# Optimization experiments

Hardware: AMD Instinct MI355X
Metric: run time of the kernel (lower is better)

Reference implementation:

```python
import jax, jax.numpy as jnp
import numpy as np

N_VERTS = 600_000
N_TETS = 1_000_000

TRI_TABLE = np.array([
    [-1,-1,-1,-1,-1,-1],[1,0,2,-1,-1,-1],[4,0,3,-1,-1,-1],[1,4,2,1,3,4],
    [3,1,5,-1,-1,-1],[2,3,0,2,5,3],[1,4,0,1,5,4],[4,2,5,-1,-1,-1],
    [4,5,2,-1,-1,-1],[4,1,0,4,5,1],[3,2,0,3,5,2],[1,3,5,-1,-1,-1],
    [4,1,2,4,3,1],[3,0,4,-1,-1,-1],[2,0,1,-1,-1,-1],[-1,-1,-1,-1,-1,-1]], dtype=np.int32)
NUM_TRI_TABLE = np.array([0,1,1,2,1,2,2,1,1,2,2,1,2,1,1,0], dtype=np.int32)
BASE_TET_EDGES = np.array([0,1,0,2,0,3,1,2,1,3,2,3], dtype=np.int64)


def setup_inputs() -> dict:
    rng = np.random.default_rng(0)
    tet = rng.integers(0, N_VERTS, size=(N_TETS, 4), dtype=np.int64)
    # static edge-unique structure (depends only on integer connectivity)
    edges = np.sort(tet[:, BASE_TET_EDGES].reshape(-1, 2), axis=1)  # (T*6, 2)
    uniq, inv = np.unique(edges, axis=0, return_inverse=True)
    key = jax.random.key(0)
    k1, k2 = jax.random.split(key)
    pos_nx3 = jax.random.normal(k1, (N_VERTS, 3), dtype=jnp.float32)
    sdf_n = jax.random.normal(k2, (N_VERTS,), dtype=jnp.float32)
    return {
        'pos_nx3': pos_nx3,
        'sdf_n': sdf_n,
        'tet_fx4': jnp.asarray(tet, dtype=jnp.int32),
        'unique_edges': jnp.asarray(uniq, dtype=jnp.int32),
        'idx_map': jnp.asarray(inv.reshape(-1, 6), dtype=jnp.int32),
    }


def reference(pos_nx3, sdf_n, tet_fx4, unique_edges, idx_map):
    tri_table = jnp.asarray(TRI_TABLE)
    num_tri_table = jnp.asarray(NUM_TRI_TABLE)
    T = tet_fx4.shape[0]

    occ_n = sdf_n > 0.0                              # (N,)
    occ_fx4 = occ_n[tet_fx4]                         # (T,4)
    occ_sum = occ_fx4.sum(-1)                        # (T,)
    valid = (occ_sum > 0) & (occ_sum < 4)            # (T,) surface tets

    # --- per-unique-edge interpolation (padded: all edges, masked) ---
    e_occ = occ_n[unique_edges]                      # (Eu,2)
    crossing = e_occ[:, 0] != e_occ[:, 1]            # sign change on edge
    s = sdf_n[unique_edges]                          # (Eu,2)
    p = pos_nx3[unique_edges]                        # (Eu,2,3)
    denom = s[:, 0] - s[:, 1]
    denom = jnp.where(crossing, denom, jnp.ones_like(denom))
    w0 = -s[:, 1] / denom                            # weight for endpoint 0
    w1 = s[:, 0] / denom                             # weight for endpoint 1
    verts = p[:, 0] * w0[:, None] + p[:, 1] * w1[:, None]
    verts = jnp.where(crossing[:, None], verts, jnp.zeros_like(verts))  # (Eu,3)

    # --- triangle table lookup (faces index the full unique-edge array) ---
    v_id = jnp.array([1, 2, 4, 8], dtype=jnp.int32)
    tetindex = (occ_fx4.astype(jnp.int32) * v_id).sum(-1)      # (T,) in [0,16)
    n_tri = num_tri_table[tetindex]                            # (T,) 0/1/2
    tri = tri_table[tetindex]                                  # (T,6) local edge ids, -1 pad
    face_idx = jnp.take_along_axis(idx_map, jnp.clip(tri, 0, 5), axis=1)
    face_idx = face_idx.reshape(T, 2, 3)
    tri_valid = valid[:, None] & (jnp.arange(2, dtype=jnp.int32)[None, :] < n_tri[:, None])
    faces = jnp.where(tri_valid[..., None], face_idx, -1)      # (T,2,3)

    # --- UV atlas (map_uv), static size ---
    Ngrid = int(np.ceil(np.sqrt((2 * T + 1) // 2)))
    lin = jnp.linspace(0.0, 1.0 - 1.0 / Ngrid, Ngrid, dtype=jnp.float32)
    tex_y, tex_x = jnp.meshgrid(lin, lin, indexing='ij')
    pad = 0.9 / Ngrid
    uvs = jnp.stack([tex_x, tex_y, tex_x + pad, tex_y,
                     tex_x + pad, tex_y + pad, tex_x, tex_y + pad], axis=-1).reshape(-1, 2)
    tet_gidx = jnp.arange(T, dtype=jnp.int32)
    tet_idx = (tet_gidx % Ngrid) + (tet_gidx // Ngrid) * Ngrid  # _idx()
    tri_i = jnp.arange(2, dtype=jnp.int32)[None, :]
    base = tet_idx[:, None] * 4                                 # (T,1)
    uv_idx = jnp.stack([jnp.broadcast_to(base, (T, 2)),
                        base + tri_i + 1,
                        base + tri_i + 2], axis=-1)             # (T,2,3)
    uv_idx = jnp.where(tri_valid[..., None], uv_idx, -1)
    return verts, faces, uvs, uv_idx
```

## Files before the change

### kernel.cpp

```cpp
#include <hip/hip_runtime.h>
#include <math.h>

__constant__ int c_tri_table[16][6] = {
    {-1,-1,-1,-1,-1,-1},{1,0,2,-1,-1,-1},{4,0,3,-1,-1,-1},{1,4,2,1,3,4},
    {3,1,5,-1,-1,-1},{2,3,0,2,5,3},{1,4,0,1,5,4},{4,2,5,-1,-1,-1},
    {4,5,2,-1,-1,-1},{4,1,0,4,5,1},{3,2,0,3,5,2},{1,3,5,-1,-1,-1},
    {4,1,2,4,3,1},{3,0,4,-1,-1,-1},{2,0,1,-1,-1,-1},{-1,-1,-1,-1,-1,-1}};
__constant__ int c_num_tri[16] = {0,1,1,2,1,2,2,1,1,2,2,1,2,1,1,0};

__global__ void dmtet_verts_kernel(const float* __restrict__ pos,
                                   const float* __restrict__ sdf,
                                   const int2* __restrict__ edges,
                                   float* __restrict__ verts, int Eu) {
    int stride = gridDim.x * blockDim.x;
    for (int e = blockIdx.x * blockDim.x + threadIdx.x; e < Eu; e += stride) {
        int2 ed = edges[e];
        float s0 = sdf[ed.x];
        float s1 = sdf[ed.y];
        bool crossing = (s0 > 0.0f) != (s1 > 0.0f);
        float denom = crossing ? (s0 - s1) : 1.0f;
        float w0 = -s1 / denom;
        float w1 =  s0 / denom;
        const float* p0 = pos + 3LL * ed.x;
        const float* p1 = pos + 3LL * ed.y;
        float ox = crossing ? (p0[0] * w0 + p1[0] * w1) : 0.0f;
        float oy = crossing ? (p0[1] * w0 + p1[1] * w1) : 0.0f;
        float oz = crossing ? (p0[2] * w0 + p1[2] * w1) : 0.0f;
        long long o = 3LL * e;
        verts[o + 0] = ox;
        verts[o + 1] = oy;
        verts[o + 2] = oz;
    }
}

__global__ void dmtet_tets_kernel(const float* __restrict__ sdf,
                                  const int4* __restrict__ tets,
                                  const int2* __restrict__ idx_map,
                                  float* __restrict__ faces_out,
                                  float* __restrict__ uvidx_out, int T) {
    int stride = gridDim.x * blockDim.x;
    for (int t = blockIdx.x * blockDim.x + threadIdx.x; t < T; t += stride) {
        int4 v = tets[t];
        int idx = (sdf[v.x] > 0.0f ? 1 : 0) | (sdf[v.y] > 0.0f ? 2 : 0) |
                  (sdf[v.z] > 0.0f ? 4 : 0) | (sdf[v.w] > 0.0f ? 8 : 0);
        int  ntri  = c_num_tri[idx];
        bool valid = (idx != 0) && (idx != 15);

        int2 a = idx_map[3LL * t + 0];
        int2 b = idx_map[3LL * t + 1];
        int2 c = idx_map[3LL * t + 2];
        int im[6] = {a.x, a.y, b.x, b.y, c.x, c.y};

        long long o = 6LL * t;
        #pragma unroll
        for (int j = 0; j < 6; ++j) {
            bool tv = valid && ((j < 3) ? (ntri > 0) : (ntri > 1));
            int tri = c_tri_table[idx][j];
            int cl = tri < 0 ? 0 : tri;
            faces_out[o + j] = (float)(tv ? im[cl] : -1);
        }

        int base = 4 * t;
        bool tv0 = valid && (ntri > 0);
        bool tv1 = valid && (ntri > 1);
        uvidx_out[o + 0] = tv0 ? (float)(base)     : -1.0f;
        uvidx_out[o + 1] = tv0 ? (float)(base + 1) : -1.0f;
        uvidx_out[o + 2] = tv0 ? (float)(base + 2) : -1.0f;
        uvidx_out[o + 3] = tv1 ? (float)(base)     : -1.0f;
        uvidx_out[o + 4] = tv1 ? (float)(base + 2) : -1.0f;
        uvidx_out[o + 5] = tv1 ? (float)(base + 3) : -1.0f;
    }
}

__global__ void dmtet_uvs_kernel(float2* __restrict__ uvs, int Ngrid,
                                 int total, float step, float pad) {
    int stride = gridDim.x * blockDim.x;
    for (int k = blockIdx.x * blockDim.x + threadIdx.x; k < total; k += stride) {
        int q = k >> 2;
        int j = k & 3;
        int gx = q % Ngrid;
        int gy = q / Ngrid;
        float x = (float)gx * step;
        float y = (float)gy * step;
        float u = (j == 1 || j == 2) ? x + pad : x;
        float w = (j >= 2) ? y + pad : y;
        uvs[k] = make_float2(u, w);
    }
}

extern "C" void kernel_launch(void* const* d_in, const int* in_sizes, int n_in,
                              void* d_out, int out_size, void* d_ws, size_t ws_size,
                              hipStream_t stream) {
    const float* pos     = (const float*)d_in[0];
    const float* sdf     = (const float*)d_in[1];
    const int*   tet     = (const int*)d_in[2];
    const int*   edges   = (const int*)d_in[3];
    const int*   idx_map = (const int*)d_in[4];

    int T  = in_sizes[2] / 4;
    int Eu = in_sizes[3] / 2;

    long long half = (2LL * T + 1) / 2;
    int Ngrid = (int)ceil(sqrt((double)half));
    while ((long long)Ngrid * Ngrid < half) Ngrid++;
    while ((long long)(Ngrid - 1) * (Ngrid - 1) >= half) Ngrid--;

    float* out   = (float*)d_out;
    float* verts = out;
    float* faces = verts + 3LL * Eu;
    float* uvs   = faces + 6LL * T;
    float* uvidx = uvs   + 8LL * Ngrid * Ngrid;

    float step = (float)((1.0 - 1.0 / (double)Ngrid) / (double)(Ngrid - 1));
    float pad  = 0.9f / (float)Ngrid;

    const int BLK = 256;
    auto nblk = [&](long long n) {
        long long b = (n + BLK - 1) / BLK;
        return (int)(b > 16384 ? 16384 : b);
    };

    dmtet_verts_kernel<<<nblk(Eu), BLK, 0, stream>>>(
        pos, sdf, (const int2*)edges, verts, Eu);

    dmtet_tets_kernel<<<nblk(T), BLK, 0, stream>>>(
        sdf, (const int4*)tet, (const int2*)idx_map, faces, uvidx, T);

    int total_uv = Ngrid * Ngrid * 4;
    dmtet_uvs_kernel<<<nblk(total_uv), BLK, 0, stream>>>(
        (float2*)uvs, Ngrid, total_uv, step, pad);
}
```

Baseline: 349.8 us.

## Vectorize loads and stores, add nontemporal hints, two edges per thread

The vertex kernel now handles two edges per thread with a 16-byte edge load and computes one reciprocal per edge instead of two divides. The tet kernel loads idx_map as one 16-byte plus one 8-byte access. The UV kernel writes 16-byte float4 values. All streaming loads and stores use nontemporal builtins, and the grid-stride loops become one-shot launches. The goal is fewer memory instructions and less cache pollution on a bandwidth-bound workload. The risks are slightly different rounding from the reciprocal multiply and a possible alignment problem on the v2i load of idx_map.

```diff
diff --git a/kernel.cpp b/kernel.cpp
--- a/kernel.cpp
+++ b/kernel.cpp
@@ -1,5 +1,10 @@
 #include <hip/hip_runtime.h>
 #include <math.h>
+
+typedef int   v2i __attribute__((ext_vector_type(2)));
+typedef int   v4i __attribute__((ext_vector_type(4)));
+typedef float v2f __attribute__((ext_vector_type(2)));
+typedef float v4f __attribute__((ext_vector_type(4)));
 
 __constant__ int c_tri_table[16][6] = {
     {-1,-1,-1,-1,-1,-1},{1,0,2,-1,-1,-1},{4,0,3,-1,-1,-1},{1,4,2,1,3,4},
@@ -8,84 +13,117 @@
     {4,1,2,4,3,1},{3,0,4,-1,-1,-1},{2,0,1,-1,-1,-1},{-1,-1,-1,-1,-1,-1}};
 __constant__ int c_num_tri[16] = {0,1,1,2,1,2,2,1,1,2,2,1,2,1,1,0};
 
-__global__ void dmtet_verts_kernel(const float* __restrict__ pos,
-                                   const float* __restrict__ sdf,
-                                   const int2* __restrict__ edges,
-                                   float* __restrict__ verts, int Eu) {
-    int stride = gridDim.x * blockDim.x;
-    for (int e = blockIdx.x * blockDim.x + threadIdx.x; e < Eu; e += stride) {
-        int2 ed = edges[e];
-        float s0 = sdf[ed.x];
-        float s1 = sdf[ed.y];
-        bool crossing = (s0 > 0.0f) != (s1 > 0.0f);
-        float denom = crossing ? (s0 - s1) : 1.0f;
-        float w0 = -s1 / denom;
-        float w1 =  s0 / denom;
-        const float* p0 = pos + 3LL * ed.x;
-        const float* p1 = pos + 3LL * ed.y;
-        float ox = crossing ? (p0[0] * w0 + p1[0] * w1) : 0.0f;
-        float oy = crossing ? (p0[1] * w0 + p1[1] * w1) : 0.0f;
-        float oz = crossing ? (p0[2] * w0 + p1[2] * w1) : 0.0f;
-        long long o = 3LL * e;
-        verts[o + 0] = ox;
-        verts[o + 1] = oy;
-        verts[o + 2] = oz;
+__global__ void __launch_bounds__(256) dmtet_verts_kernel(
+        const float* __restrict__ pos,
+        const float* __restrict__ sdf,
+        const int* __restrict__ edges,
+        float* __restrict__ verts, int Eu) {
+    int t = blockIdx.x * blockDim.x + threadIdx.x;
+    int e0 = 2 * t;
+    if (e0 >= Eu) return;
+
+    int ax, ay, bx, by;
+    bool have2 = (e0 + 1 < Eu);
+    if (have2) {
+        v4i ed = __builtin_nontemporal_load((const v4i*)(edges + 2 * e0));
+        ax = ed.x; ay = ed.y; bx = ed.z; by = ed.w;
+    } else {
+        v2i ed = __builtin_nontemporal_load((const v2i*)(edges + 2 * e0));
+        ax = ed.x; ay = ed.y; bx = ed.x; by = ed.y;
+    }
+
+    float sa0 = sdf[ax], sa1 = sdf[ay];
+    float sb0 = sdf[bx], sb1 = sdf[by];
+    const float* pa0 = pos + 3LL * ax;
+    const float* pa1 = pos + 3LL * ay;
+    const float* pb0 = pos + 3LL * bx;
+    const float* pb1 = pos + 3LL * by;
+    float a0x = pa0[0], a0y = pa0[1], a0z = pa0[2];
+    float a1x = pa1[0], a1y = pa1[1], a1z = pa1[2];
+    float b0x = pb0[0], b0y = pb0[1], b0z = pb0[2];
+    float b1x = pb1[0], b1y = pb1[1], b1z = pb1[2];
+
+    bool ca = (sa0 > 0.0f) != (sa1 > 0.0f);
+    float da = ca ? (sa0 - sa1) : 1.0f;
+    float ia = 1.0f / da;
+    float wa0 = -sa1 * ia, wa1 = sa0 * ia;
+    float ox0 = ca ? (a0x * wa0 + a1x * wa1) : 0.0f;
+    float oy0 = ca ? (a0y * wa0 + a1y * wa1) : 0.0f;
+    float oz0 = ca ? (a0z * wa0 + a1z * wa1) : 0.0f;
+
+    bool cb = (sb0 > 0.0f) != (sb1 > 0.0f);
+    float db = cb ? (sb0 - sb1) : 1.0f;
+    float ib = 1.0f / db;
+    float wb0 = -sb1 * ib, wb1 = sb0 * ib;
+    float ox1 = cb ? (b0x * wb0 + b1x * wb1) : 0.0f;
+    float oy1 = cb ? (b0y * wb0 + b1y * wb1) : 0.0f;
+    float oz1 = cb ? (b0z * wb0 + b1z * wb1) : 0.0f;
+
+    float* o = verts + 3LL * e0;
+    __builtin_nontemporal_store(ox0, o + 0);
+    __builtin_nontemporal_store(oy0, o + 1);
+    __builtin_nontemporal_store(oz0, o + 2);
+    if (have2) {
+        __builtin_nontemporal_store(ox1, o + 3);
+        __builtin_nontemporal_store(oy1, o + 4);
+        __builtin_nontemporal_store(oz1, o + 5);
     }
 }
 
-__global__ void dmtet_tets_kernel(const float* __restrict__ sdf,
-                                  const int4* __restrict__ tets,
-                                  const int2* __restrict__ idx_map,
-                                  float* __restrict__ faces_out,
-                                  float* __restrict__ uvidx_out, int T) {
-    int stride = gridDim.x * blockDim.x;
-    for (int t = blockIdx.x * blockDim.x + threadIdx.x; t < T; t += stride) {
-        int4 v = tets[t];
-        int idx = (sdf[v.x] > 0.0f ? 1 : 0) | (sdf[v.y] > 0.0f ? 2 : 0) |
-                  (sdf[v.z] > 0.0f ? 4 : 0) | (sdf[v.w] > 0.0f ? 8 : 0);
-        int  ntri  = c_num_tri[idx];
-        bool valid = (idx != 0) && (idx != 15);
+__global__ void __launch_bounds__(256) dmtet_tets_kernel(
+        const float* __restrict__ sdf,
+        const int* __restrict__ tets,
+        const int* __restrict__ idx_map,
+        float* __restrict__ faces_out,
+        float* __restrict__ uvidx_out, int T) {
+    int t = blockIdx.x * blockDim.x + threadIdx.x;
+    if (t >= T) return;
 
-        int2 a = idx_map[3LL * t + 0];
-        int2 b = idx_map[3LL * t + 1];
-        int2 c = idx_map[3LL * t + 2];
-        int im[6] = {a.x, a.y, b.x, b.y, c.x, c.y};
+    v4i v = __builtin_nontemporal_load((const v4i*)(tets + 4LL * t));
+    v4i m0 = __builtin_nontemporal_load((const v4i*)(idx_map + 6LL * t));
+    v2i m1 = __builtin_nontemporal_load((const v2i*)(idx_map + 6LL * t + 4));
 
-        long long o = 6LL * t;
-        #pragma unroll
-        for (int j = 0; j < 6; ++j) {
-            bool tv = valid && ((j < 3) ? (ntri > 0) : (ntri > 1));
-            int tri = c_tri_table[idx][j];
-            int cl = tri < 0 ? 0 : tri;
-            faces_out[o + j] = (float)(tv ? im[cl] : -1);
-        }
+    int idx = (sdf[v.x] > 0.0f ? 1 : 0) | (sdf[v.y] > 0.0f ? 2 : 0) |
+              (sdf[v.z] > 0.0f ? 4 : 0) | (sdf[v.w] > 0.0f ? 8 : 0);
+    int  ntri  = c_num_tri[idx];
+    bool valid = (idx != 0) && (idx != 15);
 
-        int base = 4 * t;
-        bool tv0 = valid && (ntri > 0);
-        bool tv1 = valid && (ntri > 1);
-        uvidx_out[o + 0] = tv0 ? (float)(base)     : -1.0f;
-        uvidx_out[o + 1] = tv0 ? (float)(base + 1) : -1.0f;
-        uvidx_out[o + 2] = tv0 ? (float)(base + 2) : -1.0f;
-        uvidx_out[o + 3] = tv1 ? (float)(base)     : -1.0f;
-        uvidx_out[o + 4] = tv1 ? (float)(base + 2) : -1.0f;
-        uvidx_out[o + 5] = tv1 ? (float)(base + 3) : -1.0f;
+    int im[6] = {m0.x, m0.y, m0.z, m0.w, m1.x, m1.y};
+
+    long long o = 6LL * t;
+    #pragma unroll
+    for (int j = 0; j < 6; ++j) {
+        bool tv = valid && ((j < 3) ? (ntri > 0) : (ntri > 1));
+        int tri = c_tri_table[idx][j];
+        int cl = tri < 0 ? 0 : tri;
+        __builtin_nontemporal_store((float)(tv ? im[cl] : -1), faces_out + o + j);
     }
+
+    int base = 4 * t;
+    bool tv0 = valid && (ntri > 0);
+    bool tv1 = valid && (ntri > 1);
+    __builtin_nontemporal_store(tv0 ? (float)(base)     : -1.0f, uvidx_out + o + 0);
+    __builtin_nontemporal_store(tv0 ? (float)(base + 1) : -1.0f, uvidx_out + o + 1);
+    __builtin_nontemporal_store(tv0 ? (float)(base + 2) : -1.0f, uvidx_out + o + 2);
+    __builtin_nontemporal_store(tv1 ? (float)(base)     : -1.0f, uvidx_out + o + 3);
+    __builtin_nontemporal_store(tv1 ? (float)(base + 2) : -1.0f, uvidx_out + o + 4);
+    __builtin_nontemporal_store(tv1 ? (float)(base + 3) : -1.0f, uvidx_out + o + 5);
 }
 
-__global__ void dmtet_uvs_kernel(float2* __restrict__ uvs, int Ngrid,
-                                 int total, float step, float pad) {
-    int stride = gridDim.x * blockDim.x;
-    for (int k = blockIdx.x * blockDim.x + threadIdx.x; k < total; k += stride) {
-        int q = k >> 2;
-        int j = k & 3;
-        int gx = q % Ngrid;
-        int gy = q / Ngrid;
-        float x = (float)gx * step;
-        float y = (float)gy * step;
-        float u = (j == 1 || j == 2) ? x + pad : x;
-        float w = (j >= 2) ? y + pad : y;
-        uvs[k] = make_float2(u, w);
-    }
+__global__ void __launch_bounds__(256) dmtet_uvs_kernel(
+        v4f* __restrict__ uvs, int Ngrid, int npairs, float step, float pad) {
+    int k = blockIdx.x * blockDim.x + threadIdx.x;
+    if (k >= npairs) return;
+    int q = k >> 1;
+    int h = k & 1;
+    int gx = q % Ngrid;
+    int gy = q / Ngrid;
+    float x = (float)gx * step;
+    float y = (float)gy * step;
+    v4f out;
+    if (h == 0) { out.x = x;       out.y = y;       out.z = x + pad; out.w = y; }
+    else        { out.x = x + pad; out.y = y + pad; out.z = x;       out.w = y + pad; }
+    __builtin_nontemporal_store(out, uvs + k);
 }
 
 extern "C" void kernel_launch(void* const* d_in, const int* in_sizes, int n_in,
@@ -115,18 +153,15 @@
     float pad  = 0.9f / (float)Ngrid;
 
     const int BLK = 256;
-    auto nblk = [&](long long n) {
-        long long b = (n + BLK - 1) / BLK;
-        return (int)(b > 16384 ? 16384 : b);
-    };
 
-    dmtet_verts_kernel<<<nblk(Eu), BLK, 0, stream>>>(
-        pos, sdf, (const int2*)edges, verts, Eu);
+    int vthreads = (Eu + 1) / 2;
+    dmtet_verts_kernel<<<(vthreads + BLK - 1) / BLK, BLK, 0, stream>>>(
+        pos, sdf, edges, verts, Eu);
 
-    dmtet_tets_kernel<<<nblk(T), BLK, 0, stream>>>(
-        sdf, (const int4*)tet, (const int2*)idx_map, faces, uvidx, T);
+    dmtet_tets_kernel<<<(T + BLK - 1) / BLK, BLK, 0, stream>>>(
+        sdf, tet, idx_map, faces, uvidx, T);
 
-    int total_uv = Ngrid * Ngrid * 4;
-    dmtet_uvs_kernel<<<nblk(total_uv), BLK, 0, stream>>>(
-        (float2*)uvs, Ngrid, total_uv, step, pad);
+    int npairs = Ngrid * Ngrid * 2;
+    dmtet_uvs_kernel<<<(npairs + BLK - 1) / BLK, BLK, 0, stream>>>(
+        (v4f*)uvs, Ngrid, npairs, step, pad);
 }
```

Measured after the change: 369.3 us. 1.06x slower.
